# Kernel optimization log

Hardware: AMD Instinct MI355X
Metric: run time of the kernel (lower is better)

The kernel has to match this reference:

```python
import jax, jax.numpy as jnp
import numpy as np
from jax import lax

A, T, B, OBS, H, ACT = 4, 128, 256, 128, 128, 8  # agents, time, envs, obs_dim, gru_hidden(=embed), act_dim


def setup_inputs() -> dict:
    key = jax.random.key(0)
    ks = jax.random.split(key, 16)
    def w(k, shape, fan_in):
        return (jax.random.normal(k, shape, jnp.float32) / np.float32(np.sqrt(fan_in)))
    return {
        "hstate": jnp.zeros((A, B, H), jnp.float32),
        "obs": jax.random.normal(ks[0], (A, T, B, OBS), jnp.float32),
        "avail_actions": jnp.ones((A, T, B, ACT), jnp.float32),
        # embedding dense
        "We": w(ks[1], (A, OBS, H), OBS), "be": jnp.zeros((A, H), jnp.float32),
        # GRU: input kernels (r|z|n concat) with bias, hidden kernels (r|z|n), only n-hidden has bias
        "Wi": w(ks[2], (A, H, 3 * H), H), "bi": jnp.zeros((A, 3 * H), jnp.float32),
        "Wh": w(ks[3], (A, H, 3 * H), H), "bhn": jnp.zeros((A, H), jnp.float32),
        # actor head
        "Wa1": w(ks[4], (A, H, H), H), "ba1": jnp.zeros((A, H), jnp.float32),
        "Wa2": 0.01 * w(ks[5], (A, H, ACT), H), "ba2": jnp.zeros((A, ACT), jnp.float32),
        "log_std": jnp.zeros((A, ACT), jnp.float32),
        # critic head
        "Wc1": w(ks[6], (A, H, H), H), "bc1": jnp.zeros((A, H), jnp.float32),
        "Wc2": w(ks[7], (A, H, 1), H), "bc2": jnp.zeros((A, 1), jnp.float32),
        "done": jax.random.bernoulli(ks[8], 0.05, (A, T, B)),
    }


def _agent_forward(h0, obs, done, avail_actions, We, be, Wi, bi, Wh, bhn,
                   Wa1, ba1, Wa2, ba2, log_std, Wc1, bc1, Wc2, bc2):
    # obs: [T,B,OBS], done: [T,B], h0: [B,H]
    act = jnp.tanh  # config['network']['activation'] == 'tanh'
    emb = act(jnp.einsum('tbo,oh->tbh', obs, We) + be)          # [T,B,H]
    xi = jnp.einsum('tbh,hg->tbg', emb, Wi) + bi                # [T,B,3H] precomputed input gates

    def step(h, xs):
        xi_t, d = xs                                            # [B,3H], [B]
        h = jnp.where(d[:, None], 0.0, h)                       # reset on done
        hh = h @ Wh                                             # [B,3H]
        xr, xz, xn = jnp.split(xi_t, 3, axis=-1)
        hr, hz, hn = jnp.split(hh, 3, axis=-1)
        r = jax.nn.sigmoid(xr + hr)
        z = jax.nn.sigmoid(xz + hz)
        n = jnp.tanh(xn + r * (hn + bhn))
        h_new = (1.0 - z) * n + z * h
        return h_new, h_new

    hT, ys = lax.scan(step, h0, (xi, done))                     # ys: [T,B,H]
    a = act(jnp.einsum('tbh,hk->tbk', ys, Wa1) + ba1)
    mean = jnp.einsum('tbh,ha->tba', a, Wa2) + ba2              # [T,B,ACT]
    std = jnp.exp(log_std)                                      # [ACT]
    c = act(jnp.einsum('tbh,hk->tbk', ys, Wc1) + bc1)
    value = (jnp.einsum('tbh,ho->tbo', c, Wc2) + bc2)[..., 0]   # [T,B]
    return hT, mean, std, value


def reference(hstate, obs, avail_actions, We, be, Wi, bi, Wh, bhn,
              Wa1, ba1, Wa2, ba2, log_std, Wc1, bc1, Wc2, bc2, done):
    hT, mean, std, value = jax.vmap(_agent_forward)(
        hstate, obs, done, avail_actions, We, be, Wi, bi, Wh, bhn,
        Wa1, ba1, Wa2, ba2, log_std, Wc1, bc1, Wc2, bc2)
    return hT, mean, std, value
```

## Files before the change

kernel.cpp:

```cpp
#include <hip/hip_runtime.h>

typedef unsigned short u16;
typedef __attribute__((ext_vector_type(8))) short short8;
typedef __attribute__((ext_vector_type(4))) float f32x4;

#define A_ 4
#define T_ 128
#define B_ 256
#define OBS_ 128
#define H_ 128
#define G_ 384
#define ACT_ 8

__device__ __forceinline__ u16 f2b(float x) {
    unsigned int u = __float_as_uint(x);
    u = (u + 0x7fffu + ((u >> 16) & 1u)) >> 16;
    return (u16)u;
}
__device__ __forceinline__ u16 f2bc(float x) {
    return (u16)((__float_as_uint(x) + 0x8000u) >> 16);
}
__device__ __forceinline__ float b2f(u16 h) {
    return __uint_as_float(((unsigned int)h) << 16);
}
__device__ __forceinline__ float fexp2_(float x) { return __builtin_amdgcn_exp2f(x); }
__device__ __forceinline__ float frcp_(float x) { return __builtin_amdgcn_rcpf(x); }
__device__ __forceinline__ float sigmoidf_(float x) {
    return frcp_(1.0f + fexp2_(-1.4426950408889634f * x));
}
__device__ __forceinline__ float tanhf_(float x) {
    return 1.0f - 2.0f * frcp_(1.0f + fexp2_(2.8853900817779268f * x));
}
__device__ __forceinline__ f32x4 mfma16(short8 a, short8 b, f32x4 c) {
    return __builtin_amdgcn_mfma_f32_16x16x32_bf16(a, b, c, 0, 0, 0);
}

__global__ void k_prep(const float* __restrict__ We, const float* __restrict__ Wi,
                       const float* __restrict__ Wh, const float* __restrict__ Wa1,
                       const float* __restrict__ Wc1, const float* __restrict__ Wa2,
                       const float* __restrict__ Wc2, const float* __restrict__ log_std,
                       u16* __restrict__ weT, u16* __restrict__ wiT, u16* __restrict__ whT,
                       u16* __restrict__ wa1T, u16* __restrict__ wc1T, u16* __restrict__ h2T,
                       float* __restrict__ std_out) {
    const int PER_A = 149504;
    int idx = blockIdx.x * 256 + threadIdx.x;
    const int total = 4 * PER_A;
    if (idx < total) {
        int a = idx / PER_A;
        int i = idx % PER_A;
        if (i < 16384) {
            int h = i >> 7, o = i & 127;
            weT[a * 16384 + i] = f2b(We[a * 16384 + o * 128 + h]);
        } else if (i < 16384 + 49152) {
            int j = i - 16384; int g = j >> 7, k = j & 127;
            wiT[a * 49152 + j] = f2b(Wi[a * 49152 + k * 384 + g]);
        } else if (i < 16384 + 2 * 49152) {
            int j = i - 16384 - 49152; int g = j >> 7, k = j & 127;
            whT[a * 49152 + j] = f2b(Wh[a * 49152 + k * 384 + g]);
        } else if (i < 2 * 16384 + 2 * 49152) {
            int j = i - 16384 - 2 * 49152; int h2 = j >> 7, k = j & 127;
            wa1T[a * 16384 + j] = f2b(Wa1[a * 16384 + k * 128 + h2]);
        } else if (i < 3 * 16384 + 2 * 49152) {
            int j = i - 2 * 16384 - 2 * 49152; int h2 = j >> 7, k = j & 127;
            wc1T[a * 16384 + j] = f2b(Wc1[a * 16384 + k * 128 + h2]);
        } else {
            int j = i - 3 * 16384 - 2 * 49152; int row = j >> 7, k = j & 127;
            float v = 0.f;
            if (row < 8) v = Wa2[a * 1024 + k * 8 + row];
            else if (row == 8) v = Wc2[a * 128 + k];
            h2T[a * 2048 + j] = f2b(v);
        }
    } else if (idx < total + 32) {
        int i = idx - total;
        std_out[i] = __expf(log_std[i]);
    }
}

__global__ __launch_bounds__(512) void k_embed_xi(
    const float* __restrict__ obs, const float* __restrict__ be, const float* __restrict__ bi,
    const u16* __restrict__ weT, const u16* __restrict__ wiT, u16* __restrict__ xi_ws) {
    __shared__ __align__(16) u16 obsl[16][136];
    __shared__ __align__(16) u16 elds[16][136];
    const int a = blockIdx.y, t = blockIdx.x;
    const int wid = threadIdx.x >> 6, lane = threadIdx.x & 63;
    const int m = lane & 15, quad = lane >> 4;
    const int srow = threadIdx.x >> 5, schunk = threadIdx.x & 31;

    short8 we[4], wi[3][4];
    {
        const u16* p = weT + a * 16384 + (wid * 16 + m) * 128 + quad * 8;
#pragma unroll
        for (int ks = 0; ks < 4; ++ks) we[ks] = *(const short8*)(p + ks * 32);
#pragma unroll
        for (int g = 0; g < 3; ++g) {
            const u16* q = wiT + a * 49152 + (g * 128 + wid * 16 + m) * 128 + quad * 8;
#pragma unroll
            for (int ks = 0; ks < 4; ++ks) wi[g][ks] = *(const short8*)(q + ks * 32);
        }
    }
    const float bee = be[a * H_ + wid * 16 + m];
    float big[3];
#pragma unroll
    for (int g = 0; g < 3; ++g) big[g] = bi[a * G_ + g * 128 + wid * 16 + m];

    const float* obsrow = obs + ((size_t)(a * T_ + t) * B_ + srow) * OBS_ + schunk * 4;
    float4 pf = *(const float4*)(obsrow);
    ushort4* xi4 = (ushort4*)xi_ws;

    for (int it = 0; it < 16; ++it) {
        ushort4 ob;
        ob.x = f2b(pf.x); ob.y = f2b(pf.y); ob.z = f2b(pf.z); ob.w = f2b(pf.w);
        *(ushort4*)&obsl[srow][schunk * 4] = ob;
        __syncthreads();
        if (it + 1 < 16) pf = *(const float4*)(obsrow + (size_t)(it + 1) * 2048);

        short8 af[4];
#pragma unroll
        for (int ks = 0; ks < 4; ++ks)
            af[ks] = *(const short8*)&obsl[m][ks * 32 + quad * 8];
        f32x4 acc = f32x4{0.f, 0.f, 0.f, 0.f};
#pragma unroll
        for (int ks = 0; ks < 4; ++ks) acc = mfma16(af[ks], we[ks], acc);
#pragma unroll
        for (int r = 0; r < 4; ++r)
            elds[quad * 4 + r][wid * 16 + m] = f2b(tanhf_(acc[r] + bee));
        __syncthreads();

        short8 ef[4];
#pragma unroll
        for (int ks = 0; ks < 4; ++ks)
            ef[ks] = *(const short8*)&elds[m][ks * 32 + quad * 8];
        f32x4 xa[3];
#pragma unroll
        for (int g = 0; g < 3; ++g) xa[g] = f32x4{0.f, 0.f, 0.f, 0.f};
#pragma unroll
        for (int ks = 0; ks < 4; ++ks)
#pragma unroll
            for (int g = 0; g < 3; ++g) xa[g] = mfma16(ef[ks], wi[g][ks], xa[g]);

        const size_t base = ((size_t)(a * 16 + it) * T_ + t) * 1536;
#pragma unroll
        for (int g = 0; g < 3; ++g) {
            ushort4 pk;
            pk.x = f2b(xa[g][0] + big[g]);
            pk.y = f2b(xa[g][1] + big[g]);
            pk.z = f2b(xa[g][2] + big[g]);
            pk.w = f2b(xa[g][3] + big[g]);
            xi4[base + (size_t)(wid * 3 + g) * 64 + lane] = pk;
        }
    }
}

__global__ __launch_bounds__(512, 2) void k_scan(
    const float* __restrict__ hstate, const u16* __restrict__ xi_ws,
    const u16* __restrict__ whT, const float* __restrict__ bhn,
    const int* __restrict__ done,
    const u16* __restrict__ wa1T, const u16* __restrict__ wc1T, const u16* __restrict__ h2T,
    const float* __restrict__ ba1, const float* __restrict__ bc1,
    const float* __restrict__ ba2, const float* __restrict__ bc2,
    float* __restrict__ hT_out, float* __restrict__ mean_out, float* __restrict__ val_out) {
    __shared__ __align__(16) u16 hlds[2][16][136];
    __shared__ __align__(16) u16 al[2][2][16][136];
    const int a = blockIdx.y, btile = blockIdx.x;
    const int wid = threadIdx.x >> 6, lane = threadIdx.x & 63;
    const int m = lane & 15, quad = lane >> 4;
    const int b0 = btile * 16;
    const int col = 16 * wid + m;

    short8 wh[3][4];
    const u16* whTa = whT + a * 49152;
#pragma unroll
    for (int g = 0; g < 3; ++g) {
        const u16* p = whTa + (g * 128 + col) * 128 + quad * 8;
#pragma unroll
        for (int ks = 0; ks < 4; ++ks) wh[g][ks] = *(const short8*)(p + ks * 32);
    }
    short8 wa[4], wc[4], h2f[4];
    {
        const u16* pa = wa1T + a * 16384 + col * 128 + quad * 8;
        const u16* pc = wc1T + a * 16384 + col * 128 + quad * 8;
        const u16* ph = h2T + a * 2048 + m * 128 + quad * 8;
#pragma unroll
        for (int ks = 0; ks < 4; ++ks) {
            wa[ks] = *(const short8*)(pa + ks * 32);
            wc[ks] = *(const short8*)(pc + ks * 32);
            h2f[ks] = *(const short8*)(ph + ks * 32);
        }
    }
    const float bh = bhn[a * H_ + col];
    const float fa = ba1[a * 128 + col];
    const float fc = bc1[a * 128 + col];
    float bb2 = 0.f;
    if (wid == 0) { if (m < 8) bb2 = ba2[a * 8 + m]; }
    else if (wid == 1) { if (m == 8) bb2 = bc2[a]; }

    float hm[4]; u16 hb[4];
#pragma unroll
    for (int r = 0; r < 4; ++r) {
        float v = hstate[((size_t)a * B_ + b0 + quad * 4 + r) * H_ + col];
        hm[r] = v; hb[r] = f2b(v);
    }

    const ushort4* xi4 = (const ushort4*)xi_ws;
    const size_t xibase = ((size_t)(a * 16 + btile) * T_) * 1536 + wid * 192 + lane;
    const int* dptr = done + (size_t)a * T_ * B_ + b0 + quad * 4;
    const int* dAq = done + (size_t)a * T_ * B_ + b0 + m;

    ushort4 px0 = xi4[xibase], px1 = xi4[xibase + 64], px2 = xi4[xibase + 128];
    int4 dn = *(const int4*)(dptr);
    int dead = dAq[0];

    for (int t = 0; t < T_; ++t) {
        u16 (*hl)[136] = hlds[t & 1];
#pragma unroll
        for (int r = 0; r < 4; ++r) hl[quad * 4 + r][col] = hb[r];
        if (dn.x) hm[0] = 0.f;
        if (dn.y) hm[1] = 0.f;
        if (dn.z) hm[2] = 0.f;
        if (dn.w) hm[3] = 0.f;
        __syncthreads();

        f32x4 ar, az, an;
        float xn[4];
        ar[0] = b2f(px0.x); ar[1] = b2f(px0.y); ar[2] = b2f(px0.z); ar[3] = b2f(px0.w);
        az[0] = b2f(px1.x); az[1] = b2f(px1.y); az[2] = b2f(px1.z); az[3] = b2f(px1.w);
        xn[0] = b2f(px2.x); xn[1] = b2f(px2.y); xn[2] = b2f(px2.z); xn[3] = b2f(px2.w);
        an = f32x4{0.f, 0.f, 0.f, 0.f};
        const int deadcur = dead;
        if (t + 1 < T_) {
            const size_t nx = xibase + (size_t)(t + 1) * 1536;
            px0 = xi4[nx]; px1 = xi4[nx + 64]; px2 = xi4[nx + 128];
            dn = *(const int4*)(dptr + (size_t)(t + 1) * B_);
            dead = dAq[(size_t)(t + 1) * B_];
        }

        short8 af[4];
#pragma unroll
        for (int ks = 0; ks < 4; ++ks)
            af[ks] = *(const short8*)&hl[m][ks * 32 + quad * 8];

        f32x4 aa, ac;
        if (t > 0) {
            aa = f32x4{fa, fa, fa, fa};
            ac = f32x4{fc, fc, fc, fc};
#pragma unroll
            for (int ks = 0; ks < 4; ++ks) {
                aa = mfma16(af[ks], wa[ks], aa);
                ac = mfma16(af[ks], wc[ks], ac);
            }
        }

        const short8 z8 = short8{0, 0, 0, 0, 0, 0, 0, 0};
        short8 afr[4];
#pragma unroll
        for (int ks = 0; ks < 4; ++ks) afr[ks] = deadcur ? z8 : af[ks];
#pragma unroll
        for (int ks = 0; ks < 4; ++ks) {
            ar = mfma16(afr[ks], wh[0][ks], ar);
            az = mfma16(afr[ks], wh[1][ks], az);
            an = mfma16(afr[ks], wh[2][ks], an);
        }

        if (t > 0) {
#pragma unroll
            for (int r = 0; r < 4; ++r) {
                al[t & 1][0][quad * 4 + r][col] = f2b(tanhf_(aa[r]));
                al[t & 1][1][quad * 4 + r][col] = f2b(tanhf_(ac[r]));
            }
            __syncthreads();
        }

#pragma unroll
        for (int r = 0; r < 4; ++r) {
            const float rg = sigmoidf_(ar[r]);
            const float zg = sigmoidf_(az[r]);
            const float ng = tanhf_(fmaf(rg, an[r] + bh, xn[r]));
            const float hn2 = fmaf(zg, hm[r] - ng, ng);
            hm[r] = hn2;
            hb[r] = f2bc(hn2);
        }

        if (t > 0 && wid < 2) {
            short8 tf[4];
#pragma unroll
            for (int ks = 0; ks < 4; ++ks)
                tf[ks] = *(const short8*)&al[t & 1][wid][m][ks * 32 + quad * 8];
            f32x4 tacc = f32x4{bb2, bb2, bb2, bb2};
#pragma unroll
            for (int ks = 0; ks < 4; ++ks) tacc = mfma16(tf[ks], h2f[ks], tacc);
            const size_t R0 = (size_t)a * 32768 + (size_t)(t - 1) * 256 + b0;
            if (wid == 0) {
                if (m < 8) {
#pragma unroll
                    for (int r = 0; r < 4; ++r)
                        mean_out[(R0 + quad * 4 + r) * 8 + m] = tacc[r];
                }
            } else {
                if (m == 8) {
#pragma unroll
                    for (int r = 0; r < 4; ++r)
                        val_out[R0 + quad * 4 + r] = tacc[r];
                }
            }
        }
    }

#pragma unroll
    for (int r = 0; r < 4; ++r)
        hT_out[((size_t)a * B_ + b0 + quad * 4 + r) * H_ + col] = hm[r];

    {
        u16 (*hl)[136] = hlds[0];
#pragma unroll
        for (int r = 0; r < 4; ++r) hl[quad * 4 + r][col] = hb[r];
        __syncthreads();
        short8 af[4];
#pragma unroll
        for (int ks = 0; ks < 4; ++ks)
            af[ks] = *(const short8*)&hl[m][ks * 32 + quad * 8];
        f32x4 aa = f32x4{fa, fa, fa, fa};
        f32x4 ac = f32x4{fc, fc, fc, fc};
#pragma unroll
        for (int ks = 0; ks < 4; ++ks) {
            aa = mfma16(af[ks], wa[ks], aa);
            ac = mfma16(af[ks], wc[ks], ac);
        }
#pragma unroll
        for (int r = 0; r < 4; ++r) {
            al[0][0][quad * 4 + r][col] = f2b(tanhf_(aa[r]));
            al[0][1][quad * 4 + r][col] = f2b(tanhf_(ac[r]));
        }
        __syncthreads();
        if (wid < 2) {
            short8 tf[4];
#pragma unroll
            for (int ks = 0; ks < 4; ++ks)
                tf[ks] = *(const short8*)&al[0][wid][m][ks * 32 + quad * 8];
            f32x4 tacc = f32x4{bb2, bb2, bb2, bb2};
#pragma unroll
            for (int ks = 0; ks < 4; ++ks) tacc = mfma16(tf[ks], h2f[ks], tacc);
            const size_t R0 = (size_t)a * 32768 + (size_t)(T_ - 1) * 256 + b0;
            if (wid == 0) {
                if (m < 8) {
#pragma unroll
                    for (int r = 0; r < 4; ++r)
                        mean_out[(R0 + quad * 4 + r) * 8 + m] = tacc[r];
                }
            } else {
                if (m == 8) {
#pragma unroll
                    for (int r = 0; r < 4; ++r)
                        val_out[R0 + quad * 4 + r] = tacc[r];
                }
            }
        }
    }
}

extern "C" void kernel_launch(void* const* d_in, const int* in_sizes, int n_in,
                              void* d_out, int out_size, void* d_ws, size_t ws_size,
                              hipStream_t stream) {
    const float* hstate = (const float*)d_in[0];
    const float* obs = (const float*)d_in[1];
    const float* We = (const float*)d_in[3];
    const float* be = (const float*)d_in[4];
    const float* Wi = (const float*)d_in[5];
    const float* bi = (const float*)d_in[6];
    const float* Wh = (const float*)d_in[7];
    const float* bhn = (const float*)d_in[8];
    const float* Wa1 = (const float*)d_in[9];
    const float* ba1 = (const float*)d_in[10];
    const float* Wa2 = (const float*)d_in[11];
    const float* ba2 = (const float*)d_in[12];
    const float* log_std = (const float*)d_in[13];
    const float* Wc1 = (const float*)d_in[14];
    const float* bc1 = (const float*)d_in[15];
    const float* Wc2 = (const float*)d_in[16];
    const float* bc2 = (const float*)d_in[17];
    const int* done = (const int*)d_in[18];

    float* out = (float*)d_out;
    float* hT_out = out;
    float* mean_out = out + 131072;
    float* std_out = out + 1179648;
    float* val_out = out + 1179680;

    u16* ws = (u16*)d_ws;
    u16* xi = ws;
    u16* ys = xi + 50331648;
    u16* weT = ys + 16777216;
    u16* wiT = weT + 65536;
    u16* whT = wiT + 196608;
    u16* wa1T = whT + 196608;
    u16* wc1T = wa1T + 65536;
    u16* h2T = wc1T + 65536;

    hipLaunchKernelGGL(k_prep, dim3(2337), dim3(256), 0, stream,
                       We, Wi, Wh, Wa1, Wc1, Wa2, Wc2, log_std,
                       weT, wiT, whT, wa1T, wc1T, h2T, std_out);
    hipLaunchKernelGGL(k_embed_xi, dim3(128, 4), dim3(512), 0, stream,
                       obs, be, bi, weT, wiT, xi);
    hipLaunchKernelGGL(k_scan, dim3(16, 4), dim3(512), 0, stream,
                       hstate, xi, whT, bhn, done,
                       wa1T, wc1T, h2T, ba1, bc1, ba2, bc2,
                       hT_out, mean_out, val_out);
}
```

Before: 317.7 us.

## Fold activation scales into weights, split embed grid, defer head projection

The sigmoid/tanh pre-scaling constants are folded into the bf16 weights and biases at prep time, and biases seed the MFMA accumulators, so the scan's inner loop saves multiplies and adds. The embed/xi kernel is split in half across a z grid dimension to double block count, with double-buffered shared memory and a software-pipelined stage that drops one barrier per iteration. In the scan, the actor/critic output projection is delayed by one more step to remove a __syncthreads, and dead-state zeroing is gated behind a wave-level any check. Scaling weights before bf16 rounding shifts rounding error slightly, and the extra pipeline stage adds epilogue code.

```diff
diff --git a/kernel.cpp b/kernel.cpp
--- a/kernel.cpp
+++ b/kernel.cpp
@@ -11,6 +11,8 @@
 #define H_ 128
 #define G_ 384
 #define ACT_ 8
+#define SIGS -1.4426950408889634f
+#define TANS 2.8853900817779268f
 
 __device__ __forceinline__ u16 f2b(float x) {
     unsigned int u = __float_as_uint(x);
@@ -25,11 +27,9 @@
 }
 __device__ __forceinline__ float fexp2_(float x) { return __builtin_amdgcn_exp2f(x); }
 __device__ __forceinline__ float frcp_(float x) { return __builtin_amdgcn_rcpf(x); }
-__device__ __forceinline__ float sigmoidf_(float x) {
-    return frcp_(1.0f + fexp2_(-1.4426950408889634f * x));
-}
-__device__ __forceinline__ float tanhf_(float x) {
-    return 1.0f - 2.0f * frcp_(1.0f + fexp2_(2.8853900817779268f * x));
+__device__ __forceinline__ float sig_pre(float x) { return frcp_(1.0f + fexp2_(x)); }
+__device__ __forceinline__ float tanh_pre(float x) {
+    return fmaf(-2.0f, frcp_(1.0f + fexp2_(x)), 1.0f);
 }
 __device__ __forceinline__ f32x4 mfma16(short8 a, short8 b, f32x4 c) {
     return __builtin_amdgcn_mfma_f32_16x16x32_bf16(a, b, c, 0, 0, 0);
@@ -50,19 +50,21 @@
         int i = idx % PER_A;
         if (i < 16384) {
             int h = i >> 7, o = i & 127;
-            weT[a * 16384 + i] = f2b(We[a * 16384 + o * 128 + h]);
+            weT[a * 16384 + i] = f2b(TANS * We[a * 16384 + o * 128 + h]);
         } else if (i < 16384 + 49152) {
             int j = i - 16384; int g = j >> 7, k = j & 127;
-            wiT[a * 49152 + j] = f2b(Wi[a * 49152 + k * 384 + g]);
+            float s = (g < 256) ? SIGS : TANS;
+            wiT[a * 49152 + j] = f2b(s * Wi[a * 49152 + k * 384 + g]);
         } else if (i < 16384 + 2 * 49152) {
             int j = i - 16384 - 49152; int g = j >> 7, k = j & 127;
-            whT[a * 49152 + j] = f2b(Wh[a * 49152 + k * 384 + g]);
+            float s = (g < 256) ? SIGS : TANS;
+            whT[a * 49152 + j] = f2b(s * Wh[a * 49152 + k * 384 + g]);
         } else if (i < 2 * 16384 + 2 * 49152) {
             int j = i - 16384 - 2 * 49152; int h2 = j >> 7, k = j & 127;
-            wa1T[a * 16384 + j] = f2b(Wa1[a * 16384 + k * 128 + h2]);
+            wa1T[a * 16384 + j] = f2b(TANS * Wa1[a * 16384 + k * 128 + h2]);
         } else if (i < 3 * 16384 + 2 * 49152) {
             int j = i - 2 * 16384 - 2 * 49152; int h2 = j >> 7, k = j & 127;
-            wc1T[a * 16384 + j] = f2b(Wc1[a * 16384 + k * 128 + h2]);
+            wc1T[a * 16384 + j] = f2b(TANS * Wc1[a * 16384 + k * 128 + h2]);
         } else {
             int j = i - 3 * 16384 - 2 * 49152; int row = j >> 7, k = j & 127;
             float v = 0.f;
@@ -79,9 +81,9 @@
 __global__ __launch_bounds__(512) void k_embed_xi(
     const float* __restrict__ obs, const float* __restrict__ be, const float* __restrict__ bi,
     const u16* __restrict__ weT, const u16* __restrict__ wiT, u16* __restrict__ xi_ws) {
-    __shared__ __align__(16) u16 obsl[16][136];
-    __shared__ __align__(16) u16 elds[16][136];
-    const int a = blockIdx.y, t = blockIdx.x;
+    __shared__ __align__(16) u16 obsl[2][16][136];
+    __shared__ __align__(16) u16 elds[2][16][136];
+    const int a = blockIdx.y, t = blockIdx.x, half = blockIdx.z;
     const int wid = threadIdx.x >> 6, lane = threadIdx.x & 63;
     const int m = lane & 15, quad = lane >> 4;
     const int srow = threadIdx.x >> 5, schunk = threadIdx.x & 31;
@@ -98,54 +100,86 @@
             for (int ks = 0; ks < 4; ++ks) wi[g][ks] = *(const short8*)(q + ks * 32);
         }
     }
-    const float bee = be[a * H_ + wid * 16 + m];
+    const float bee = TANS * be[a * H_ + wid * 16 + m];
     float big[3];
 #pragma unroll
-    for (int g = 0; g < 3; ++g) big[g] = bi[a * G_ + g * 128 + wid * 16 + m];
-
-    const float* obsrow = obs + ((size_t)(a * T_ + t) * B_ + srow) * OBS_ + schunk * 4;
-    float4 pf = *(const float4*)(obsrow);
+    for (int g = 0; g < 3; ++g)
+        big[g] = ((g < 2) ? SIGS : TANS) * bi[a * G_ + g * 128 + wid * 16 + m];
+
+    const float* obsrow = obs + ((size_t)(a * T_ + t) * B_ + half * 128 + srow) * OBS_ + schunk * 4;
     ushort4* xi4 = (ushort4*)xi_ws;
 
-    for (int it = 0; it < 16; ++it) {
+    {
+        float4 p0 = *(const float4*)(obsrow);
         ushort4 ob;
-        ob.x = f2b(pf.x); ob.y = f2b(pf.y); ob.z = f2b(pf.z); ob.w = f2b(pf.w);
-        *(ushort4*)&obsl[srow][schunk * 4] = ob;
+        ob.x = f2b(p0.x); ob.y = f2b(p0.y); ob.z = f2b(p0.z); ob.w = f2b(p0.w);
+        *(ushort4*)&obsl[0][srow][schunk * 4] = ob;
+    }
+    float4 pf = *(const float4*)(obsrow + 2048);
+    __syncthreads();
+
+    for (int it = 0; it < 8; ++it) {
+        short8 af[4];
+#pragma unroll
+        for (int ks = 0; ks < 4; ++ks)
+            af[ks] = *(const short8*)&obsl[it & 1][m][ks * 32 + quad * 8];
+        if (it + 1 < 8) {
+            ushort4 ob;
+            ob.x = f2b(pf.x); ob.y = f2b(pf.y); ob.z = f2b(pf.z); ob.w = f2b(pf.w);
+            *(ushort4*)&obsl[(it + 1) & 1][srow][schunk * 4] = ob;
+            if (it + 2 < 8) pf = *(const float4*)(obsrow + (size_t)(it + 2) * 2048);
+        }
+
+        f32x4 acc = f32x4{bee, bee, bee, bee};
+#pragma unroll
+        for (int ks = 0; ks < 4; ++ks) acc = mfma16(af[ks], we[ks], acc);
+#pragma unroll
+        for (int r = 0; r < 4; ++r)
+            elds[it & 1][quad * 4 + r][wid * 16 + m] = f2bc(tanh_pre(acc[r]));
+
+        if (it > 0) {
+            short8 ef[4];
+#pragma unroll
+            for (int ks = 0; ks < 4; ++ks)
+                ef[ks] = *(const short8*)&elds[(it - 1) & 1][m][ks * 32 + quad * 8];
+            f32x4 xa[3];
+#pragma unroll
+            for (int g = 0; g < 3; ++g) xa[g] = f32x4{big[g], big[g], big[g], big[g]};
+#pragma unroll
+            for (int ks = 0; ks < 4; ++ks)
+#pragma unroll
+                for (int g = 0; g < 3; ++g) xa[g] = mfma16(ef[ks], wi[g][ks], xa[g]);
+            const int itg = half * 8 + it - 1;
+            const size_t base = ((size_t)(a * 16 + itg) * T_ + t) * 1536;
+#pragma unroll
+            for (int g = 0; g < 3; ++g) {
+                ushort4 pk;
+                pk.x = f2bc(xa[g][0]); pk.y = f2bc(xa[g][1]);
+                pk.z = f2bc(xa[g][2]); pk.w = f2bc(xa[g][3]);
+                xi4[base + (size_t)(wid * 3 + g) * 64 + lane] = pk;
+            }
+        }
         __syncthreads();
-        if (it + 1 < 16) pf = *(const float4*)(obsrow + (size_t)(it + 1) * 2048);
-
-        short8 af[4];
+    }
+    {
+        short8 ef[4];
 #pragma unroll
         for (int ks = 0; ks < 4; ++ks)
-            af[ks] = *(const short8*)&obsl[m][ks * 32 + quad * 8];
-        f32x4 acc = f32x4{0.f, 0.f, 0.f, 0.f};
-#pragma unroll
-        for (int ks = 0; ks < 4; ++ks) acc = mfma16(af[ks], we[ks], acc);
-#pragma unroll
-        for (int r = 0; r < 4; ++r)
-            elds[quad * 4 + r][wid * 16 + m] = f2b(tanhf_(acc[r] + bee));
-        __syncthreads();
-
-        short8 ef[4];
+            ef[ks] = *(const short8*)&elds[1][m][ks * 32 + quad * 8];
+        f32x4 xa[3];
+#pragma unroll
+        for (int g = 0; g < 3; ++g) xa[g] = f32x4{big[g], big[g], big[g], big[g]};
 #pragma unroll
         for (int ks = 0; ks < 4; ++ks)
-            ef[ks] = *(const short8*)&elds[m][ks * 32 + quad * 8];
-        f32x4 xa[3];
-#pragma unroll
-        for (int g = 0; g < 3; ++g) xa[g] = f32x4{0.f, 0.f, 0.f, 0.f};
-#pragma unroll
-        for (int ks = 0; ks < 4; ++ks)
 #pragma unroll
             for (int g = 0; g < 3; ++g) xa[g] = mfma16(ef[ks], wi[g][ks], xa[g]);
-
-        const size_t base = ((size_t)(a * 16 + it) * T_ + t) * 1536;
+        const int itg = half * 8 + 7;
+        const size_t base = ((size_t)(a * 16 + itg) * T_ + t) * 1536;
 #pragma unroll
         for (int g = 0; g < 3; ++g) {
             ushort4 pk;
-            pk.x = f2b(xa[g][0] + big[g]);
-            pk.y = f2b(xa[g][1] + big[g]);
-            pk.z = f2b(xa[g][2] + big[g]);
-            pk.w = f2b(xa[g][3] + big[g]);
+            pk.x = f2bc(xa[g][0]); pk.y = f2bc(xa[g][1]);
+            pk.z = f2bc(xa[g][2]); pk.w = f2bc(xa[g][3]);
             xi4[base + (size_t)(wid * 3 + g) * 64 + lane] = pk;
         }
     }
@@ -187,9 +221,9 @@
             h2f[ks] = *(const short8*)(ph + ks * 32);
         }
     }
-    const float bh = bhn[a * H_ + col];
-    const float fa = ba1[a * 128 + col];
-    const float fc = bc1[a * 128 + col];
+    const float bh = TANS * bhn[a * H_ + col];
+    const float fa = TANS * ba1[a * 128 + col];
+    const float fc = TANS * bc1[a * 128 + col];
     float bb2 = 0.f;
     if (wid == 0) { if (m < 8) bb2 = ba2[a * 8 + m]; }
     else if (wid == 1) { if (m == 8) bb2 = bc2[a]; }
@@ -225,7 +259,7 @@
         ar[0] = b2f(px0.x); ar[1] = b2f(px0.y); ar[2] = b2f(px0.z); ar[3] = b2f(px0.w);
         az[0] = b2f(px1.x); az[1] = b2f(px1.y); az[2] = b2f(px1.z); az[3] = b2f(px1.w);
         xn[0] = b2f(px2.x); xn[1] = b2f(px2.y); xn[2] = b2f(px2.z); xn[3] = b2f(px2.w);
-        an = f32x4{0.f, 0.f, 0.f, 0.f};
+        an = f32x4{bh, bh, bh, bh};
         const int deadcur = dead;
         if (t + 1 < T_) {
             const size_t nx = xibase + (size_t)(t + 1) * 1536;
@@ -250,10 +284,14 @@
             }
         }
 
-        const short8 z8 = short8{0, 0, 0, 0, 0, 0, 0, 0};
         short8 afr[4];
 #pragma unroll
-        for (int ks = 0; ks < 4; ++ks) afr[ks] = deadcur ? z8 : af[ks];
+        for (int ks = 0; ks < 4; ++ks) afr[ks] = af[ks];
+        if (__any(deadcur)) {
+            const short8 z8 = short8{0, 0, 0, 0, 0, 0, 0, 0};
+#pragma unroll
+            for (int ks = 0; ks < 4; ++ks) if (deadcur) afr[ks] = z8;
+        }
 #pragma unroll
         for (int ks = 0; ks < 4; ++ks) {
             ar = mfma16(afr[ks], wh[0][ks], ar);
@@ -264,31 +302,30 @@
         if (t > 0) {
 #pragma unroll
             for (int r = 0; r < 4; ++r) {
-                al[t & 1][0][quad * 4 + r][col] = f2b(tanhf_(aa[r]));
-                al[t & 1][1][quad * 4 + r][col] = f2b(tanhf_(ac[r]));
-            }
-            __syncthreads();
+                al[t & 1][0][quad * 4 + r][col] = f2bc(tanh_pre(aa[r]));
+                al[t & 1][1][quad * 4 + r][col] = f2bc(tanh_pre(ac[r]));
+            }
         }
 
 #pragma unroll
         for (int r = 0; r < 4; ++r) {
-            const float rg = sigmoidf_(ar[r]);
-            const float zg = sigmoidf_(az[r]);
-            const float ng = tanhf_(fmaf(rg, an[r] + bh, xn[r]));
+            const float rg = sig_pre(ar[r]);
+            const float zg = sig_pre(az[r]);
+            const float ng = tanh_pre(fmaf(rg, an[r], xn[r]));
             const float hn2 = fmaf(zg, hm[r] - ng, ng);
             hm[r] = hn2;
             hb[r] = f2bc(hn2);
         }
 
-        if (t > 0 && wid < 2) {
+        if (t >= 2 && wid < 2) {
             short8 tf[4];
 #pragma unroll
             for (int ks = 0; ks < 4; ++ks)
-                tf[ks] = *(const short8*)&al[t & 1][wid][m][ks * 32 + quad * 8];
+                tf[ks] = *(const short8*)&al[(t - 1) & 1][wid][m][ks * 32 + quad * 8];
             f32x4 tacc = f32x4{bb2, bb2, bb2, bb2};
 #pragma unroll
             for (int ks = 0; ks < 4; ++ks) tacc = mfma16(tf[ks], h2f[ks], tacc);
-            const size_t R0 = (size_t)a * 32768 + (size_t)(t - 1) * 256 + b0;
+            const size_t R0 = (size_t)a * 32768 + (size_t)(t - 2) * 256 + b0;
             if (wid == 0) {
                 if (m < 8) {
 #pragma unroll
@@ -327,8 +364,31 @@
         }
 #pragma unroll
         for (int r = 0; r < 4; ++r) {
-            al[0][0][quad * 4 + r][col] = f2b(tanhf_(aa[r]));
-            al[0][1][quad * 4 + r][col] = f2b(tanhf_(ac[r]));
+            al[0][0][quad * 4 + r][col] = f2bc(tanh_pre(aa[r]));
+            al[0][1][quad * 4 + r][col] = f2bc(tanh_pre(ac[r]));
+        }
+        if (wid < 2) {
+            short8 tf[4];
+#pragma unroll
+            for (int ks = 0; ks < 4; ++ks)
+                tf[ks] = *(const short8*)&al[1][wid][m][ks * 32 + quad * 8];
+            f32x4 tacc = f32x4{bb2, bb2, bb2, bb2};
+#pragma unroll
+            for (int ks = 0; ks < 4; ++ks) tacc = mfma16(tf[ks], h2f[ks], tacc);
+            const size_t R0 = (size_t)a * 32768 + (size_t)(T_ - 2) * 256 + b0;
+            if (wid == 0) {
+                if (m < 8) {
+#pragma unroll
+                    for (int r = 0; r < 4; ++r)
+                        mean_out[(R0 + quad * 4 + r) * 8 + m] = tacc[r];
+                }
+            } else {
+                if (m == 8) {
+#pragma unroll
+                    for (int r = 0; r < 4; ++r)
+                        val_out[R0 + quad * 4 + r] = tacc[r];
+                }
+            }
         }
         __syncthreads();
         if (wid < 2) {
@@ -398,7 +458,7 @@
     hipLaunchKernelGGL(k_prep, dim3(2337), dim3(256), 0, stream,
                        We, Wi, Wh, Wa1, Wc1, Wa2, Wc2, log_std,
                        weT, wiT, whT, wa1T, wc1T, h2T, std_out);
-    hipLaunchKernelGGL(k_embed_xi, dim3(128, 4), dim3(512), 0, stream,
+    hipLaunchKernelGGL(k_embed_xi, dim3(128, 4, 2), dim3(512), 0, stream,
                        obs, be, bi, weT, wiT, xi);
     hipLaunchKernelGGL(k_scan, dim3(16, 4), dim3(512), 0, stream,
                        hstate, xi, whT, bhn, done,
```

New measurement: 302.7 us. 4.7% less time.
